# Kernel optimization log

Measured on AMD Instinct MI355X. Metric: run time of the kernel, lower is better.

Reference implementation:

```python
import jax, jax.numpy as jnp
import numpy as np

BLOCK = (4, 4, 4)
NUM_HEADS = 8


def setup_inputs() -> dict:
    key = jax.random.key(0)
    ks = jax.random.split(key, 5)
    C = 128
    return {
        "x": jax.random.normal(ks[0], (2, C, 32, 62, 62), dtype=jnp.float32),
        "qkv_w": jax.random.normal(ks[1], (3 * C, C), dtype=jnp.float32) * 0.02,
        "qkv_b": jax.random.normal(ks[2], (3 * C,), dtype=jnp.float32) * 0.02,
        "conv_w": jax.random.normal(ks[3], (C, C, 1, 1, 1), dtype=jnp.float32) * 0.02,
        "conv_b": jax.random.normal(ks[4], (C,), dtype=jnp.float32) * 0.02,
    }


def reference(x, qkv_w, qkv_b, conv_w, conv_b):
    b0, b1, b2 = BLOCK
    heads = NUM_HEADS
    B, C, D, H0, W0 = x.shape
    pad_r = (-W0) % b2
    pad_b = (-H0) % b1
    x = jnp.pad(x, ((0, 0), (0, 0), (0, 0), (0, pad_b), (0, pad_r)))
    H, W = H0 + pad_b, W0 + pad_r
    d, h, w = D // b0, H // b1, W // b2
    hd = C // heads
    scale = hd ** (-0.5)
    T = b0 * b1 * b2  # tokens per 3D window
    nw = d * h * w    # number of windows

    # partition into windows: (B, nw, T, C)
    xw = x.reshape(B, C, d, b0, h, b1, w, b2).transpose(0, 2, 4, 6, 3, 5, 7, 1)
    xw = xw.reshape(B, nw, T, C)

    qkv = xw @ qkv_w.T + qkv_b  # (B, nw, T, 3C)
    qkv = qkv.reshape(B, nw, T, 3, heads, hd).transpose(3, 0, 1, 4, 2, 5)
    q, k, v = qkv[0], qkv[1], qkv[2]  # (B, nw, heads, T, hd)

    attn = jnp.einsum('bnhtc,bnhsc->bnhts', q, k) * scale

    if pad_r > 0 or pad_b > 0:
        mask = jnp.zeros((H, W), dtype=attn.dtype)
        if pad_b > 0:
            mask = mask.at[-pad_b:, :].set(1.0)
        if pad_r > 0:
            mask = mask.at[:, -pad_r:].set(1.0)
        # (h*w, b1*b2) per-2D-window pad flags
        mask = mask.reshape(h, b1, w, b2).transpose(0, 2, 1, 3).reshape(h * w, b1 * b2)
        am = mask[:, None, :] - mask[:, :, None]  # (h*w, b1*b2, b1*b2)
        am = jnp.where(am != 0, jnp.asarray(-1000.0, attn.dtype), jnp.asarray(0.0, attn.dtype))
        # tile over depth windows and depth tokens (matches torch .repeat)
        am = jnp.tile(am, (d, b0, b0))  # (nw, T, T)
        attn = attn + am[None, :, None, :, :]

    attn = jax.nn.softmax(attn, axis=-1)
    o = jnp.einsum('bnhts,bnhsc->bnhtc', attn, v)  # (B, nw, heads, T, hd)

    o = o.reshape(B, d, h, w, heads, b0, b1, b2, hd)
    o = o.transpose(0, 4, 8, 1, 5, 2, 6, 3, 7).reshape(B, C, D, H, W)
    o = o[:, :, :, :H0, :W0]

    # 1x1x1 Conv3d == channel mixing
    out = jnp.einsum('bcdhw,oc->bodhw', o, conv_w[:, :, 0, 0, 0])
    out = out + conv_b[None, :, None, None, None]
    return out
```

## Files before the change

kernel.cpp:

```cpp
#include <hip/hip_runtime.h>

typedef _Float16 f16x8 __attribute__((ext_vector_type(8)));
typedef _Float16 f16x4 __attribute__((ext_vector_type(4)));
typedef __fp16   fp16x2 __attribute__((ext_vector_type(2)));
typedef float    f32x4 __attribute__((ext_vector_type(4)));
typedef unsigned int u32x2 __attribute__((ext_vector_type(2)));

__device__ __forceinline__ f32x4 mfma32(f16x8 a, f16x8 b, f32x4 c) {
  return __builtin_amdgcn_mfma_f32_16x16x32_f16(a, b, c, 0, 0, 0);
}
__device__ __forceinline__ f32x4 mfma16(f16x4 a, f16x4 b, f32x4 c) {
#if __has_builtin(__builtin_amdgcn_mfma_f32_16x16x16f16)
  return __builtin_amdgcn_mfma_f32_16x16x16f16(a, b, c, 0, 0, 0);
#else
  f32x4 d;
  asm volatile("v_mfma_f32_16x16x16_f16 %0, %1, %2, %3"
               : "=v"(d) : "v"(a), "v"(b), "v"(c));
  return d;
#endif
}

__device__ __forceinline__ unsigned pk2(float a, float b) {
  union { fp16x2 h; unsigned u; } cv;
  cv.h = __builtin_amdgcn_cvt_pkrtz(a, b);
  return cv.u;
}

#define TR_READ(dst, addr, OFF) \
  asm volatile("ds_read_b64_tr_b16 %0, %1 offset:" OFF \
               : "=v"(dst) : "v"(addr) : "memory")

__global__ void cvt_weights(const float* __restrict__ qw, const float* __restrict__ cw,
                            _Float16* __restrict__ wq, _Float16* __restrict__ wc) {
  const int i = blockIdx.x * 256 + threadIdx.x;
  if (i < 384 * 128) wq[i] = (_Float16)qw[i];
  if (i < 128 * 128) wc[i] = (_Float16)cw[i];
}

__global__ void __launch_bounds__(512, 4)
win_attn(const float* __restrict__ xg, const _Float16* __restrict__ wq,
         const float* __restrict__ qbias, const _Float16* __restrict__ wc,
         const float* __restrict__ cb, float* __restrict__ outg)
{
  __shared__ char xsm[2][16384];
  __shared__ char wsm[8][6144];

  const int tid  = threadIdx.x;
  const int lane = tid & 63;
  const int wv   = tid >> 6;
  const int l15  = lane & 15;
  const int g    = lane >> 4;

  const int raw = blockIdx.x;
  const int wp  = ((raw & 7) << 8) | (raw >> 3);
  const int wid0 = wp * 2;
  const int ww0 = wid0 & 15, hh = (wid0 >> 4) & 15, dd = (wid0 >> 8) & 7, bb = wid0 >> 11;
  const int ww1 = ww0 + 1;

  unsigned long long pm0 = 0ull, pm1 = 0ull;
  if (hh == 15)  { pm0 |= 0xFF00FF00FF00FF00ull; pm1 |= 0xFF00FF00FF00FF00ull; }
  if (ww1 == 15)   pm1 |= 0xCCCCCCCCCCCCCCCCull;

  const f32x4 fz = {0.f, 0.f, 0.f, 0.f};
  const float LOG2E = 1.4426950408889634f;
  const int swzA = l15 << 4;
  const int vswz = (l15 & 7) << 4;

  char* sb = wsm[wv];
  const unsigned sb32 = (unsigned)(unsigned long long)sb;
  const unsigned trb  = sb32 + 8u * (unsigned)lane;

  const int m4 = lane & 3, q4 = lane >> 2;
  const int i0 = q4 >> 2, i1 = q4 & 3;
  const int z = dd * 4 + i0, y = hh * 4 + i1;
  const bool yv = (y < 62);

  auto stage_loads = [&](int wwl, float (&va)[4][4]) {
    const bool full = (wwl < 15);
#pragma unroll
    for (int it = 0; it < 4; ++it) {
      const int c = wv * 16 + it * 4 + m4;
      const float* src = xg + (((size_t)(bb * 128 + c) * 32 + (size_t)z) * 3844
                               + (size_t)(y * 62 + wwl * 4));
      float a0 = 0.f, a1 = 0.f, a2 = 0.f, a3 = 0.f;
      if (yv) {
        const float2 lo = *reinterpret_cast<const float2*>(src);
        a0 = lo.x; a1 = lo.y;
        if (full) {
          const float2 hi = *reinterpret_cast<const float2*>(src + 2);
          a2 = hi.x; a3 = hi.y;
        }
      }
      va[it][0] = a0; va[it][1] = a1; va[it][2] = a2; va[it][3] = a3;
    }
  };
  auto stage_write = [&](char* xb, float (&va)[4][4]) {
#pragma unroll
    for (int it = 0; it < 4; ++it) {
      float v0 = va[it][0], v1 = va[it][1], v2 = va[it][2], v3 = va[it][3];
      float t0 = __shfl_xor((m4 & 1) ? v0 : v1, 1);
      float t1 = __shfl_xor((m4 & 1) ? v2 : v3, 1);
      if (m4 & 1) { v0 = t0; v2 = t1; } else { v1 = t0; v3 = t1; }
      float t2 = __shfl_xor((m4 & 2) ? v0 : v2, 2);
      float t3 = __shfl_xor((m4 & 2) ? v1 : v3, 2);
      if (m4 & 2) { v0 = t2; v1 = t3; } else { v2 = t2; v3 = t3; }
      f16x4 pk; pk[0] = (_Float16)v0; pk[1] = (_Float16)v1;
                pk[2] = (_Float16)v2; pk[3] = (_Float16)v3;
      const int c0 = wv * 16 + it * 4;
      *reinterpret_cast<f16x4*>(xb + ((lane * 256 + 2 * c0) ^ ((lane & 15) << 4))) = pk;
    }
  };

  auto qkv_part1 = [&](const char* xb, f16x4 (&ka)[4], f16x4 (&qa)[4],
                       f16x8& av0, f16x8& av1) {
#pragma unroll
    for (int co = 0; co < 3; ++co) {
      f32x4 acc[4] = {fz, fz, fz, fz};
      const int col = co * 128 + wv * 16 + l15;
      __builtin_amdgcn_s_setprio(1);
#pragma unroll
      for (int kk = 0; kk < 4; ++kk) {
        const f16x8 bfr = *reinterpret_cast<const f16x8*>(wq + col * 128 + kk * 32 + g * 8);
#pragma unroll
        for (int ri = 0; ri < 4; ++ri) {
          const f16x8 a = *reinterpret_cast<const f16x8*>(
              xb + (ri * 16 + l15) * 256 + ((kk * 64 + g * 16) ^ swzA));
          acc[ri] = mfma32(a, bfr, acc[ri]);
        }
      }
      __builtin_amdgcn_s_setprio(0);
      const float bias = qbias[col];

      if (co == 2) {
#pragma unroll
        for (int ri = 0; ri < 4; ++ri) {
          const int s0 = ri * 16 + g * 4;
          *reinterpret_cast<unsigned*>(sb + 4096 + l15 * 128 + ((2 * s0) ^ vswz))
              = pk2(acc[ri][0] + bias, acc[ri][1] + bias);
          *reinterpret_cast<unsigned*>(sb + 4096 + l15 * 128 + ((2 * (s0 + 2)) ^ vswz))
              = pk2(acc[ri][2] + bias, acc[ri][3] + bias);
        }
      } else {
        const int base = (co == 0) ? 2048 : 0;
        const float sc = (co == 0) ? 0.25f : 1.0f;
#pragma unroll
        for (int ri = 0; ri < 4; ++ri) {
          const int off = ri * 512 + l15 * 32 + g * 8;
          u32x2 w;
          w[0] = pk2((acc[ri][0] + bias) * sc, (acc[ri][1] + bias) * sc);
          w[1] = pk2((acc[ri][2] + bias) * sc, (acc[ri][3] + bias) * sc);
          *reinterpret_cast<u32x2*>(sb + base + off) = w;
        }
      }
    }
    asm volatile("s_waitcnt lgkmcnt(0)" ::: "memory");

    TR_READ(ka[0], trb, "0");
    TR_READ(ka[1], trb, "512");
    TR_READ(ka[2], trb, "1024");
    TR_READ(ka[3], trb, "1536");
    TR_READ(qa[0], trb, "2048");
    TR_READ(qa[1], trb, "2560");
    TR_READ(qa[2], trb, "3072");
    TR_READ(qa[3], trb, "3584");
    av0 = *reinterpret_cast<const f16x8*>(sb + 4096 + l15 * 128 + ((g * 16) ^ vswz));
    av1 = *reinterpret_cast<const f16x8*>(sb + 4096 + l15 * 128 + ((64 + g * 16) ^ vswz));
    asm volatile("s_waitcnt lgkmcnt(0)" ::: "memory");
    __builtin_amdgcn_sched_barrier(0);
  };

  auto attn_chunks = [&](unsigned long long pm, f16x4 (&ka)[4], f16x4 (&qa)[4],
                         f16x8 av0, f16x8 av1, unsigned (&opk)[4][2]) {
#pragma unroll
    for (int tjp = 0; tjp < 2; ++tjp) {
      const int tj0 = 2 * tjp, tj1 = 2 * tjp + 1;
      f32x4 st2[4][2];
#pragma unroll
      for (int si = 0; si < 4; ++si) {
        st2[si][0] = mfma16(ka[si], qa[tj0], fz);
        st2[si][1] = mfma16(ka[si], qa[tj1], fz);
      }

      if (pm) {
#pragma unroll
        for (int tjc = 0; tjc < 2; ++tjc) {
          const int t = (2 * tjp + tjc) * 16 + l15;
          const unsigned ft = (unsigned)(pm >> t) & 1u;
#pragma unroll
          for (int si = 0; si < 4; ++si)
#pragma unroll
            for (int r = 0; r < 4; ++r) {
              const int s = si * 16 + g * 4 + r;
              const unsigned fs = (unsigned)(pm >> s) & 1u;
              if (fs != ft) st2[si][tjc][r] -= 1000.f;
            }
        }
      }

#pragma unroll
      for (int tjc = 0; tjc < 2; ++tjc) {
        float mx = st2[0][tjc][0];
#pragma unroll
        for (int si = 0; si < 4; ++si)
#pragma unroll
          for (int r = 0; r < 4; ++r) mx = fmaxf(mx, st2[si][tjc][r]);
        mx = fmaxf(mx, __shfl_xor(mx, 16));
        mx = fmaxf(mx, __shfl_xor(mx, 32));
        float sum = 0.f;
#pragma unroll
        for (int si = 0; si < 4; ++si)
#pragma unroll
          for (int r = 0; r < 4; ++r) {
            const float e = __builtin_amdgcn_exp2f((st2[si][tjc][r] - mx) * LOG2E);
            st2[si][tjc][r] = e; sum += e;
          }
        sum += __shfl_xor(sum, 16);
        sum += __shfl_xor(sum, 32);
        const float inv = __builtin_amdgcn_rcpf(sum);
#pragma unroll
        for (int si = 0; si < 4; ++si)
#pragma unroll
          for (int r = 0; r < 4; ++r) st2[si][tjc][r] *= inv;
      }

#pragma unroll
      for (int tjc = 0; tjc < 2; ++tjc) {
        const int tl = tjc * 16 + l15;
#pragma unroll
        for (int si = 0; si < 4; ++si) {
          u32x2 w;
          w[0] = pk2(st2[si][tjc][0], st2[si][tjc][1]);
          w[1] = pk2(st2[si][tjc][2], st2[si][tjc][3]);
          *reinterpret_cast<u32x2*>(sb + tl * 128 + ((si * 32 + g * 8) ^ vswz)) = w;
        }
      }
      asm volatile("s_waitcnt lgkmcnt(0)" ::: "memory");

      f32x4 oa0 = fz, oa1 = fz;
      {
        const f16x8 pa00 = *reinterpret_cast<const f16x8*>(
            sb + l15 * 128 + ((g * 16) ^ vswz));
        const f16x8 pa10 = *reinterpret_cast<const f16x8*>(
            sb + (16 + l15) * 128 + ((g * 16) ^ vswz));
        __builtin_amdgcn_s_setprio(1);
        oa0 = mfma32(av0, pa00, oa0);
        oa1 = mfma32(av0, pa10, oa1);
        const f16x8 pa01 = *reinterpret_cast<const f16x8*>(
            sb + l15 * 128 + ((64 + g * 16) ^ vswz));
        const f16x8 pa11 = *reinterpret_cast<const f16x8*>(
            sb + (16 + l15) * 128 + ((64 + g * 16) ^ vswz));
        oa0 = mfma32(av1, pa01, oa0);
        oa1 = mfma32(av1, pa11, oa1);
        __builtin_amdgcn_s_setprio(0);
      }

      if (tjp == 0) {
        opk[0][0] = pk2(oa0[0], oa0[1]); opk[0][1] = pk2(oa0[2], oa0[3]);
        opk[1][0] = pk2(oa1[0], oa1[1]); opk[1][1] = pk2(oa1[2], oa1[3]);
      } else {
        opk[2][0] = pk2(oa0[0], oa0[1]); opk[2][1] = pk2(oa0[2], oa0[3]);
        opk[3][0] = pk2(oa1[0], oa1[1]); opk[3][1] = pk2(oa1[2], oa1[3]);
      }
      __builtin_amdgcn_sched_barrier(0);
    }
  };

  auto write_o = [&](char* xb, unsigned (&opk)[4][2]) {
#pragma unroll
    for (int tj = 0; tj < 4; ++tj) {
      const int t = tj * 16 + l15;
      u32x2 w0; w0[0] = opk[tj][0]; w0[1] = opk[tj][1];
      *reinterpret_cast<u32x2*>(xb + t * 256 + ((wv * 32 + g * 8) ^ ((t & 15) << 4))) = w0;
    }
  };

  auto conv_store = [&](const char* xb, int wwl) {
    f32x4 cacc[4] = {fz, fz, fz, fz};
    const int cout = wv * 16 + l15;
    __builtin_amdgcn_s_setprio(1);
#pragma unroll
    for (int kk = 0; kk < 4; ++kk) {
      const f16x8 bfr = *reinterpret_cast<const f16x8*>(wc + cout * 128 + kk * 32 + g * 8);
#pragma unroll
      for (int ri = 0; ri < 4; ++ri) {
        const f16x8 a = *reinterpret_cast<const f16x8*>(
            xb + (ri * 16 + l15) * 256 + ((kk * 64 + g * 16) ^ swzA));
        cacc[ri] = mfma32(a, bfr, cacc[ri]);
      }
    }
    __builtin_amdgcn_s_setprio(0);
    const int yy = hh * 4 + g;
    if (yy < 62) {
      const float bias = cb[cout];
#pragma unroll
      for (int ri = 0; ri < 4; ++ri) {
        const int zz = dd * 4 + ri;
        float* dst = outg + (((size_t)(bb * 128 + cout) * 32 + (size_t)zz) * 3844
                             + (size_t)(yy * 62 + wwl * 4));
        float2 lo; lo.x = cacc[ri][0] + bias; lo.y = cacc[ri][1] + bias;
        *reinterpret_cast<float2*>(dst) = lo;
        if (wwl < 15) {
          float2 hi; hi.x = cacc[ri][2] + bias; hi.y = cacc[ri][3] + bias;
          *reinterpret_cast<float2*>(dst + 2) = hi;
        }
      }
    }
  };

  f16x4 ka[4], qa[4];
  f16x8 av0, av1;
  float va[4][4];
  unsigned opk[4][2];

  stage_loads(ww0, va);
  stage_write(xsm[0], va);
  __syncthreads();

  qkv_part1(xsm[0], ka, qa, av0, av1);
  stage_loads(ww1, va);
  attn_chunks(pm0, ka, qa, av0, av1, opk);
  __syncthreads();
  write_o(xsm[0], opk);
  stage_write(xsm[1], va);
  __syncthreads();

  conv_store(xsm[0], ww0);
  qkv_part1(xsm[1], ka, qa, av0, av1);
  attn_chunks(pm1, ka, qa, av0, av1, opk);
  __syncthreads();
  write_o(xsm[1], opk);
  __syncthreads();
  conv_store(xsm[1], ww1);
}

extern "C" void kernel_launch(void* const* d_in, const int* in_sizes, int n_in,
                              void* d_out, int out_size, void* d_ws, size_t ws_size,
                              hipStream_t stream) {
  const float* x  = (const float*)d_in[0];
  const float* qw = (const float*)d_in[1];
  const float* qb = (const float*)d_in[2];
  const float* cw = (const float*)d_in[3];
  const float* cb = (const float*)d_in[4];
  float* out = (float*)d_out;

  if (ws_size < (size_t)(384 * 128 + 128 * 128) * sizeof(_Float16)) return;
  _Float16* wq = (_Float16*)d_ws;
  _Float16* wc = wq + 384 * 128;

  cvt_weights<<<192, 256, 0, stream>>>(qw, cw, wq, wc);
  win_attn<<<2048, 512, 0, stream>>>(x, wq, qb, wc, cb, out);
}
```

Before: 172.7 us.

## Process eight windows per block with double-buffered input pipeline

Each block now loops over eight consecutive windows instead of two, with the grid cut to 512 blocks. The global load of the next window is prefetched into a second LDS buffer while the current window is computed, and the attention output goes to a dedicated LDS buffer. The log2(e) factor is folded into the Q scale, and softmax normalisation is deferred to the attention output. V is now computed first so the per-wave scratch shrinks to 4 KB. The aim is to amortise setup and keep load/compute overlap, at the cost of fewer blocks (lower occupancy and parallelism) and a serial dependency chain per block.

```diff
diff --git a/kernel.cpp b/kernel.cpp
--- a/kernel.cpp
+++ b/kernel.cpp
@@ -42,8 +42,9 @@
          const float* __restrict__ qbias, const _Float16* __restrict__ wc,
          const float* __restrict__ cb, float* __restrict__ outg)
 {
-  __shared__ char xsm[2][16384];
-  __shared__ char wsm[8][6144];
+  __shared__ char xbuf[2][16384];
+  __shared__ char obuf[16384];
+  __shared__ char wsm[8][4096];
 
   const int tid  = threadIdx.x;
   const int lane = tid & 63;
@@ -52,23 +53,20 @@
   const int g    = lane >> 4;
 
   const int raw = blockIdx.x;
-  const int wp  = ((raw & 7) << 8) | (raw >> 3);
-  const int wid0 = wp * 2;
-  const int ww0 = wid0 & 15, hh = (wid0 >> 4) & 15, dd = (wid0 >> 8) & 7, bb = wid0 >> 11;
-  const int ww1 = ww0 + 1;
-
-  unsigned long long pm0 = 0ull, pm1 = 0ull;
-  if (hh == 15)  { pm0 |= 0xFF00FF00FF00FF00ull; pm1 |= 0xFF00FF00FF00FF00ull; }
-  if (ww1 == 15)   pm1 |= 0xCCCCCCCCCCCCCCCCull;
+  const int bsw = ((raw & 7) << 6) | (raw >> 3);
+  const int wid0 = bsw * 8;
+  const int wwbase = wid0 & 15;
+  const int hh = (wid0 >> 4) & 15, dd = (wid0 >> 8) & 7, bb = wid0 >> 11;
 
   const f32x4 fz = {0.f, 0.f, 0.f, 0.f};
-  const float LOG2E = 1.4426950408889634f;
   const int swzA = l15 << 4;
   const int vswz = (l15 & 7) << 4;
 
   char* sb = wsm[wv];
   const unsigned sb32 = (unsigned)(unsigned long long)sb;
   const unsigned trb  = sb32 + 8u * (unsigned)lane;
+
+  const unsigned long long pmh = (hh == 15) ? 0xFF00FF00FF00FF00ull : 0ull;
 
   const int m4 = lane & 3, q4 = lane >> 2;
   const int i0 = q4 >> 2, i1 = q4 & 3;
@@ -111,12 +109,10 @@
     }
   };
 
-  auto qkv_part1 = [&](const char* xb, f16x4 (&ka)[4], f16x4 (&qa)[4],
-                       f16x8& av0, f16x8& av1) {
-#pragma unroll
-    for (int co = 0; co < 3; ++co) {
+  auto qkv = [&](const char* xb, f16x8& av0, f16x8& av1) {
+    {
       f32x4 acc[4] = {fz, fz, fz, fz};
-      const int col = co * 128 + wv * 16 + l15;
+      const int col = 256 + wv * 16 + l15;
       __builtin_amdgcn_s_setprio(1);
 #pragma unroll
       for (int kk = 0; kk < 4; ++kk) {
@@ -130,31 +126,51 @@
       }
       __builtin_amdgcn_s_setprio(0);
       const float bias = qbias[col];
-
-      if (co == 2) {
+#pragma unroll
+      for (int ri = 0; ri < 4; ++ri) {
+        const int s0 = ri * 16 + g * 4;
+        *reinterpret_cast<unsigned*>(sb + l15 * 128 + ((2 * s0) ^ vswz))
+            = pk2(acc[ri][0] + bias, acc[ri][1] + bias);
+        *reinterpret_cast<unsigned*>(sb + l15 * 128 + ((2 * (s0 + 2)) ^ vswz))
+            = pk2(acc[ri][2] + bias, acc[ri][3] + bias);
+      }
+    }
+    asm volatile("s_waitcnt lgkmcnt(0)" ::: "memory");
+    av0 = *reinterpret_cast<const f16x8*>(sb + l15 * 128 + ((g * 16) ^ vswz));
+    av1 = *reinterpret_cast<const f16x8*>(sb + l15 * 128 + ((64 + g * 16) ^ vswz));
+#pragma unroll
+    for (int co = 0; co < 2; ++co) {
+      f32x4 acc[4] = {fz, fz, fz, fz};
+      const int col = co * 128 + wv * 16 + l15;
+      __builtin_amdgcn_s_setprio(1);
+#pragma unroll
+      for (int kk = 0; kk < 4; ++kk) {
+        const f16x8 bfr = *reinterpret_cast<const f16x8*>(wq + col * 128 + kk * 32 + g * 8);
 #pragma unroll
         for (int ri = 0; ri < 4; ++ri) {
-          const int s0 = ri * 16 + g * 4;
-          *reinterpret_cast<unsigned*>(sb + 4096 + l15 * 128 + ((2 * s0) ^ vswz))
-              = pk2(acc[ri][0] + bias, acc[ri][1] + bias);
-          *reinterpret_cast<unsigned*>(sb + 4096 + l15 * 128 + ((2 * (s0 + 2)) ^ vswz))
-              = pk2(acc[ri][2] + bias, acc[ri][3] + bias);
-        }
-      } else {
-        const int base = (co == 0) ? 2048 : 0;
-        const float sc = (co == 0) ? 0.25f : 1.0f;
-#pragma unroll
-        for (int ri = 0; ri < 4; ++ri) {
-          const int off = ri * 512 + l15 * 32 + g * 8;
-          u32x2 w;
-          w[0] = pk2((acc[ri][0] + bias) * sc, (acc[ri][1] + bias) * sc);
-          w[1] = pk2((acc[ri][2] + bias) * sc, (acc[ri][3] + bias) * sc);
-          *reinterpret_cast<u32x2*>(sb + base + off) = w;
-        }
-      }
-    }
+          const f16x8 a = *reinterpret_cast<const f16x8*>(
+              xb + (ri * 16 + l15) * 256 + ((kk * 64 + g * 16) ^ swzA));
+          acc[ri] = mfma32(a, bfr, acc[ri]);
+        }
+      }
+      __builtin_amdgcn_s_setprio(0);
+      const float bias = qbias[col];
+      const float sc = (co == 0) ? 0.25f * 1.4426950408889634f : 1.0f;
+      const int base = (co == 0) ? 2048 : 0;
+#pragma unroll
+      for (int ri = 0; ri < 4; ++ri) {
+        const int off = ri * 512 + l15 * 32 + g * 8;
+        u32x2 w;
+        w[0] = pk2((acc[ri][0] + bias) * sc, (acc[ri][1] + bias) * sc);
+        w[1] = pk2((acc[ri][2] + bias) * sc, (acc[ri][3] + bias) * sc);
+        *reinterpret_cast<u32x2*>(sb + base + off) = w;
+      }
+    }
+  };
+
+  auto attn = [&](unsigned long long pm, f16x8 av0, f16x8 av1) {
     asm volatile("s_waitcnt lgkmcnt(0)" ::: "memory");
-
+    f16x4 ka[4], qa[4];
     TR_READ(ka[0], trb, "0");
     TR_READ(ka[1], trb, "512");
     TR_READ(ka[2], trb, "1024");
@@ -163,14 +179,9 @@
     TR_READ(qa[1], trb, "2560");
     TR_READ(qa[2], trb, "3072");
     TR_READ(qa[3], trb, "3584");
-    av0 = *reinterpret_cast<const f16x8*>(sb + 4096 + l15 * 128 + ((g * 16) ^ vswz));
-    av1 = *reinterpret_cast<const f16x8*>(sb + 4096 + l15 * 128 + ((64 + g * 16) ^ vswz));
     asm volatile("s_waitcnt lgkmcnt(0)" ::: "memory");
     __builtin_amdgcn_sched_barrier(0);
-  };
-
-  auto attn_chunks = [&](unsigned long long pm, f16x4 (&ka)[4], f16x4 (&qa)[4],
-                         f16x8 av0, f16x8 av1, unsigned (&opk)[4][2]) {
+
 #pragma unroll
     for (int tjp = 0; tjp < 2; ++tjp) {
       const int tj0 = 2 * tjp, tj1 = 2 * tjp + 1;
@@ -197,6 +208,7 @@
         }
       }
 
+      float invs[2];
 #pragma unroll
       for (int tjc = 0; tjc < 2; ++tjc) {
         float mx = st2[0][tjc][0];
@@ -211,16 +223,12 @@
         for (int si = 0; si < 4; ++si)
 #pragma unroll
           for (int r = 0; r < 4; ++r) {
-            const float e = __builtin_amdgcn_exp2f((st2[si][tjc][r] - mx) * LOG2E);
+            const float e = __builtin_amdgcn_exp2f(st2[si][tjc][r] - mx);
             st2[si][tjc][r] = e; sum += e;
           }
         sum += __shfl_xor(sum, 16);
         sum += __shfl_xor(sum, 32);
-        const float inv = __builtin_amdgcn_rcpf(sum);
-#pragma unroll
-        for (int si = 0; si < 4; ++si)
-#pragma unroll
-          for (int r = 0; r < 4; ++r) st2[si][tjc][r] *= inv;
+        invs[tjc] = __builtin_amdgcn_rcpf(sum);
       }
 
 #pragma unroll
@@ -254,27 +262,22 @@
         __builtin_amdgcn_s_setprio(0);
       }
 
-      if (tjp == 0) {
-        opk[0][0] = pk2(oa0[0], oa0[1]); opk[0][1] = pk2(oa0[2], oa0[3]);
-        opk[1][0] = pk2(oa1[0], oa1[1]); opk[1][1] = pk2(oa1[2], oa1[3]);
-      } else {
-        opk[2][0] = pk2(oa0[0], oa0[1]); opk[2][1] = pk2(oa0[2], oa0[3]);
-        opk[3][0] = pk2(oa1[0], oa1[1]); opk[3][1] = pk2(oa1[2], oa1[3]);
-      }
-      __builtin_amdgcn_sched_barrier(0);
-    }
-  };
-
-  auto write_o = [&](char* xb, unsigned (&opk)[4][2]) {
-#pragma unroll
-    for (int tj = 0; tj < 4; ++tj) {
-      const int t = tj * 16 + l15;
-      u32x2 w0; w0[0] = opk[tj][0]; w0[1] = opk[tj][1];
-      *reinterpret_cast<u32x2*>(xb + t * 256 + ((wv * 32 + g * 8) ^ ((t & 15) << 4))) = w0;
-    }
-  };
-
-  auto conv_store = [&](const char* xb, int wwl) {
+      {
+        const int t0 = tj0 * 16 + l15;
+        u32x2 w0;
+        w0[0] = pk2(oa0[0] * invs[0], oa0[1] * invs[0]);
+        w0[1] = pk2(oa0[2] * invs[0], oa0[3] * invs[0]);
+        *reinterpret_cast<u32x2*>(obuf + t0 * 256 + ((wv * 32 + g * 8) ^ ((t0 & 15) << 4))) = w0;
+        const int t1 = tj1 * 16 + l15;
+        u32x2 w1;
+        w1[0] = pk2(oa1[0] * invs[1], oa1[1] * invs[1]);
+        w1[1] = pk2(oa1[2] * invs[1], oa1[3] * invs[1]);
+        *reinterpret_cast<u32x2*>(obuf + t1 * 256 + ((wv * 32 + g * 8) ^ ((t1 & 15) << 4))) = w1;
+      }
+    }
+  };
+
+  auto conv_store = [&](int wwl) {
     f32x4 cacc[4] = {fz, fz, fz, fz};
     const int cout = wv * 16 + l15;
     __builtin_amdgcn_s_setprio(1);
@@ -284,7 +287,7 @@
 #pragma unroll
       for (int ri = 0; ri < 4; ++ri) {
         const f16x8 a = *reinterpret_cast<const f16x8*>(
-            xb + (ri * 16 + l15) * 256 + ((kk * 64 + g * 16) ^ swzA));
+            obuf + (ri * 16 + l15) * 256 + ((kk * 64 + g * 16) ^ swzA));
         cacc[ri] = mfma32(a, bfr, cacc[ri]);
       }
     }
@@ -307,30 +310,39 @@
     }
   };
 
-  f16x4 ka[4], qa[4];
+  char* pA = xbuf[0];
+  char* pB = xbuf[1];
   f16x8 av0, av1;
-  float va[4][4];
-  unsigned opk[4][2];
-
-  stage_loads(ww0, va);
-  stage_write(xsm[0], va);
+
+  {
+    float va[4][4];
+    stage_loads(wwbase + 0, va);
+    stage_write(pA, va);
+  }
   __syncthreads();
 
-  qkv_part1(xsm[0], ka, qa, av0, av1);
-  stage_loads(ww1, va);
-  attn_chunks(pm0, ka, qa, av0, av1, opk);
-  __syncthreads();
-  write_o(xsm[0], opk);
-  stage_write(xsm[1], va);
-  __syncthreads();
-
-  conv_store(xsm[0], ww0);
-  qkv_part1(xsm[1], ka, qa, av0, av1);
-  attn_chunks(pm1, ka, qa, av0, av1, opk);
-  __syncthreads();
-  write_o(xsm[1], opk);
-  __syncthreads();
-  conv_store(xsm[1], ww1);
+#pragma unroll 1
+  for (int w = 0; w < 7; ++w) {
+    const int wwl = wwbase + w;
+    {
+      float va[4][4];
+      stage_loads(wwl + 1, va);
+      qkv(pA, av0, av1);
+      stage_write(pB, va);
+    }
+    attn(pmh | ((wwl == 15) ? 0xCCCCCCCCCCCCCCCCull : 0ull), av0, av1);
+    __syncthreads();
+    conv_store(wwl);
+    __syncthreads();
+    char* tmp = pA; pA = pB; pB = tmp;
+  }
+  {
+    const int wwl = wwbase + 7;
+    qkv(pA, av0, av1);
+    attn(pmh | ((wwl == 15) ? 0xCCCCCCCCCCCCCCCCull : 0ull), av0, av1);
+    __syncthreads();
+    conv_store(wwl);
+  }
 }
 
 extern "C" void kernel_launch(void* const* d_in, const int* in_sizes, int n_in,
@@ -348,5 +360,5 @@
   _Float16* wc = wq + 384 * 128;
 
   cvt_weights<<<192, 256, 0, stream>>>(qw, cw, wq, wc);
-  win_attn<<<2048, 512, 0, stream>>>(x, wq, qb, wc, cb, out);
-}
+  win_attn<<<512, 512, 0, stream>>>(x, wq, qb, wc, cb, out);
+}
```

Measured after the change: 349.8 us. +102.6%, slower.
